# Kernel optimization log

Hardware: AMD Instinct MI355X
Metric: run time of the kernel (lower is better)

Reference implementation:

```python
import jax, jax.numpy as jnp
import numpy as np

DIM = 256      # z feature dim
HEADS = 8
C = 64         # per-head dim == x channel dim
INNER = HEADS * C  # 512


def setup_inputs() -> dict:
    key = jax.random.key(0)
    ks = jax.random.split(key, 8)
    b, h, w, m = 8, 64, 64, 256
    x = jax.random.normal(ks[0], (b, C, h, w), dtype=jnp.float32)
    z = jax.random.normal(ks[1], (b, m, DIM), dtype=jnp.float32)
    s = 1.0 / np.sqrt(DIM)
    Wk = jax.random.normal(ks[2], (DIM, INNER), dtype=jnp.float32) * s
    bk = jnp.zeros((INNER,), dtype=jnp.float32)
    Wv = jax.random.normal(ks[3], (DIM, INNER), dtype=jnp.float32) * s
    bv = jnp.zeros((INNER,), dtype=jnp.float32)
    Wo = jax.random.normal(ks[4], (INNER, C), dtype=jnp.float32) * (1.0 / np.sqrt(INNER))
    bo = jnp.zeros((C,), dtype=jnp.float32)
    return {"x": x, "z": z, "Wk": Wk, "bk": bk, "Wv": Wv, "bv": bv, "Wo": Wo, "bo": bo}


def reference(x, z, Wk, bk, Wv, bv, Wo, bo):
    b, c, h, w = x.shape
    m = z.shape[1]
    heads = Wk.shape[1] // c
    hw = h * w
    # Faithful to torch: raw view (b,c,h,w)->(b,hw,c), then repeat along feature
    # dim and raw view into (b, heads, hw, c).
    q = jnp.tile(x.reshape(b, hw, c), (1, 1, heads)).reshape(b, heads, hw, c)
    # k/v: Linear then raw view (b, m, heads*c) -> (b, heads, m, c).
    k = (z @ Wk + bk).reshape(b, heads, m, c)
    v = (z @ Wv + bv).reshape(b, heads, m, c)
    scale = c ** (-0.5)
    dots = jnp.einsum('bhlc,bhmc->bhlm', q, k) * scale
    attn = jax.nn.softmax(dots, axis=-1)
    out = jnp.einsum('bhlm,bhmc->bhlc', attn, v)
    out = jnp.transpose(out, (0, 2, 1, 3)).reshape(b, hw, heads * c)  # b l (h c)
    out = out @ Wo + bo  # (b, hw, c)
    # Faithful raw view back to (b, c, h, w), then residual.
    return x + out.reshape(b, c, h, w)
```

## Files before the change

kernel.cpp:

```cpp
#include <hip/hip_runtime.h>

#define HEADS 8
#define CH    64
#define HW    4096
#define MTOK  256
#define DIMZ  256
#define INNER 512
#define LROWS 512

typedef __attribute__((ext_vector_type(8))) __bf16 bf16x8;
typedef __attribute__((ext_vector_type(4))) float  f32x4;

__device__ __forceinline__ unsigned f2bf(float f) {
  unsigned u = __float_as_uint(f);
  return (u + 0x7fffu + ((u >> 16) & 1u)) >> 16;
}

__device__ __forceinline__ bf16x8 ld_bf8(const unsigned short* p) {
  uint4 v = *(const uint4*)p;
  return __builtin_bit_cast(bf16x8, v);
}

__device__ __forceinline__ bf16x8 cvt8(const float* p) {
  float4 f0 = *(const float4*)p;
  float4 f1 = *(const float4*)(p + 4);
  uint4 u;
  u.x = f2bf(f0.x) | (f2bf(f0.y) << 16);
  u.y = f2bf(f0.z) | (f2bf(f0.w) << 16);
  u.z = f2bf(f1.x) | (f2bf(f1.y) << 16);
  u.w = f2bf(f1.z) | (f2bf(f1.w) << 16);
  return __builtin_bit_cast(bf16x8, u);
}

__global__ __launch_bounds__(256) void kv_gen(
    const float* __restrict__ z,
    const float* __restrict__ Wk, const float* __restrict__ bk,
    const float* __restrict__ Wv, const float* __restrict__ bv,
    const float* __restrict__ Wo,
    unsigned short* __restrict__ klin, unsigned short* __restrict__ vt,
    unsigned short* __restrict__ WoT) {
  __shared__ unsigned short Tw[2][64][40];
  __shared__ float Tf[64][65];
  const int t = threadIdx.x;
  const int bn = blockIdx.y;

  if (bn == 16) {
    if (blockIdx.x >= 8) return;
    const int k0 = blockIdx.x * 64;
    const int rr = t >> 6, cc = t & 63;
#pragma unroll
    for (int it = 0; it < 16; ++it) {
      int r = it * 4 + rr;
      Tf[r][cc] = Wo[(size_t)(k0 + r) * CH + cc];
    }
    __syncthreads();
    const int nr = t >> 5, kp = t & 31;
#pragma unroll
    for (int it = 0; it < 8; ++it) {
      int n = it * 8 + nr;
      unsigned w = f2bf(Tf[kp * 2][n]) | (f2bf(Tf[kp * 2 + 1][n]) << 16);
      *(unsigned*)(WoT + (size_t)n * INNER + k0 + kp * 2) = w;
    }
    return;
  }

  const int lane = t & 63, wid = t >> 6;
  const int c = lane & 15, g = lane >> 4;
  const int mb = blockIdx.x;
  const bool isK = bn < 8;
  const int nb = bn & 7;
  const float* __restrict__ W    = isK ? Wk : Wv;
  const float* __restrict__ bias = isK ? bk : bv;
  const int m0 = mb * 64 + (wid >> 1) * 32;
  const int n0 = nb * 64 + (wid & 1) * 32;
  const int nloc = (wid & 1) * 32;
  const int skk = t >> 3, snn = (t & 7) * 8;

  f32x4 acc[2][2];
#pragma unroll
  for (int i = 0; i < 2; ++i)
#pragma unroll
    for (int j = 0; j < 2; ++j) acc[i][j] = (f32x4)0.f;

  {
    const float* wp = W + (size_t)skk * INNER + nb * 64 + snn;
    float4 w0 = *(const float4*)wp;
    float4 w1 = *(const float4*)(wp + 4);
    Tw[0][snn + 0][skk] = (unsigned short)f2bf(w0.x);
    Tw[0][snn + 1][skk] = (unsigned short)f2bf(w0.y);
    Tw[0][snn + 2][skk] = (unsigned short)f2bf(w0.z);
    Tw[0][snn + 3][skk] = (unsigned short)f2bf(w0.w);
    Tw[0][snn + 4][skk] = (unsigned short)f2bf(w1.x);
    Tw[0][snn + 5][skk] = (unsigned short)f2bf(w1.y);
    Tw[0][snn + 6][skk] = (unsigned short)f2bf(w1.z);
    Tw[0][snn + 7][skk] = (unsigned short)f2bf(w1.w);
  }
  __syncthreads();

#pragma unroll
  for (int s = 0; s < 8; ++s) {
    const int k0 = s * 32;
    if (s < 7) {
      const int nb2 = (s + 1) & 1;
      const float* wp = W + (size_t)(k0 + 32 + skk) * INNER + nb * 64 + snn;
      float4 w0 = *(const float4*)wp;
      float4 w1 = *(const float4*)(wp + 4);
      Tw[nb2][snn + 0][skk] = (unsigned short)f2bf(w0.x);
      Tw[nb2][snn + 1][skk] = (unsigned short)f2bf(w0.y);
      Tw[nb2][snn + 2][skk] = (unsigned short)f2bf(w0.z);
      Tw[nb2][snn + 3][skk] = (unsigned short)f2bf(w0.w);
      Tw[nb2][snn + 4][skk] = (unsigned short)f2bf(w1.x);
      Tw[nb2][snn + 5][skk] = (unsigned short)f2bf(w1.y);
      Tw[nb2][snn + 6][skk] = (unsigned short)f2bf(w1.z);
      Tw[nb2][snn + 7][skk] = (unsigned short)f2bf(w1.w);
    }
    const int cb = s & 1;
    bf16x8 a0 = cvt8(z + (size_t)(m0 + c) * DIMZ + k0 + 8 * g);
    bf16x8 a1 = cvt8(z + (size_t)(m0 + 16 + c) * DIMZ + k0 + 8 * g);
    bf16x8 b0 = *(const bf16x8*)&Tw[cb][nloc + c][8 * g];
    bf16x8 b1 = *(const bf16x8*)&Tw[cb][nloc + 16 + c][8 * g];
    if (isK) {
      acc[0][0] = __builtin_amdgcn_mfma_f32_16x16x32_bf16(b0, a0, acc[0][0], 0, 0, 0);
      acc[0][1] = __builtin_amdgcn_mfma_f32_16x16x32_bf16(b1, a0, acc[0][1], 0, 0, 0);
      acc[1][0] = __builtin_amdgcn_mfma_f32_16x16x32_bf16(b0, a1, acc[1][0], 0, 0, 0);
      acc[1][1] = __builtin_amdgcn_mfma_f32_16x16x32_bf16(b1, a1, acc[1][1], 0, 0, 0);
    } else {
      acc[0][0] = __builtin_amdgcn_mfma_f32_16x16x32_bf16(a0, b0, acc[0][0], 0, 0, 0);
      acc[0][1] = __builtin_amdgcn_mfma_f32_16x16x32_bf16(a0, b1, acc[0][1], 0, 0, 0);
      acc[1][0] = __builtin_amdgcn_mfma_f32_16x16x32_bf16(a1, b0, acc[1][0], 0, 0, 0);
      acc[1][1] = __builtin_amdgcn_mfma_f32_16x16x32_bf16(a1, b1, acc[1][1], 0, 0, 0);
    }
    __syncthreads();
  }

  if (isK) {
#pragma unroll
    for (int mt = 0; mt < 2; ++mt)
#pragma unroll
      for (int nt = 0; nt < 2; ++nt) {
        const int m = m0 + mt * 16 + c;
        const int n = n0 + nt * 16 + 4 * g;
        float4 b4 = *(const float4*)(bias + n);
        uint2 w;
        w.x = f2bf(acc[mt][nt][0] + b4.x) | (f2bf(acc[mt][nt][1] + b4.y) << 16);
        w.y = f2bf(acc[mt][nt][2] + b4.z) | (f2bf(acc[mt][nt][3] + b4.w) << 16);
        *(uint2*)(klin + (size_t)m * INNER + n) = w;
      }
  } else {
#pragma unroll
    for (int mt = 0; mt < 2; ++mt)
#pragma unroll
      for (int nt = 0; nt < 2; ++nt) {
        const int n = n0 + nt * 16 + c;
        const float bn1 = bias[n];
        const int m = m0 + mt * 16 + 4 * g;
        const int bb = m >> 8;
        const int mtk = m & 255;
        const int h = mtk >> 5, t0 = mtk & 31;
        const int cc2 = n & 63, cb2 = n >> 6;
        uint2 w;
        w.x = f2bf(acc[mt][nt][0] + bn1) | (f2bf(acc[mt][nt][1] + bn1) << 16);
        w.y = f2bf(acc[mt][nt][2] + bn1) | (f2bf(acc[mt][nt][3] + bn1) << 16);
        *(uint2*)(vt + ((size_t)((bb * HEADS + h) * CH + cc2)) * MTOK + cb2 * 32 + t0) = w;
      }
  }
}

__global__ __launch_bounds__(512) void attnproj(
    const float* __restrict__ x,
    const unsigned short* __restrict__ kbf,
    const unsigned short* __restrict__ vtbf,
    const unsigned short* __restrict__ WoT, const float* __restrict__ bo,
    float* __restrict__ y) {
  __shared__ __align__(16) char lds[65536 + 16384];
  char* Osh = lds + 65536;
  float* Sp = (float*)lds;
  const int t = threadIdx.x;
  const int lane = t & 63, wid = t >> 6;
  const int c = lane & 15, g = lane >> 4;
  const int bid = blockIdx.x;
  const int qc = bid & 31, b = bid >> 5;
  const int hh = wid;
  const int qbase = qc * 16;
  char* Pb = lds + wid * 8192;

  {
    const float* xs = x + (size_t)b * (HW * CH) + (size_t)hh * (LROWS * CH);
    const unsigned short* Kg = kbf + ((size_t)b * MTOK + hh * 32) * INNER;
    const unsigned short* Vg = vtbf + (size_t)(b * HEADS + hh) * (CH * MTOK);

    const float qs = 0.125f * 1.44269504089f;
    bf16x8 qfr[2];
#pragma unroll
    for (int ks = 0; ks < 2; ++ks) {
      const float* qp = xs + (size_t)(qbase + c) * CH + 32 * ks + 8 * g;
      float4 f0 = *(const float4*)qp;
      float4 f1 = *(const float4*)(qp + 4);
      uint4 u;
      u.x = f2bf(f0.x * qs) | (f2bf(f0.y * qs) << 16);
      u.y = f2bf(f0.z * qs) | (f2bf(f0.w * qs) << 16);
      u.z = f2bf(f1.x * qs) | (f2bf(f1.y * qs) << 16);
      u.w = f2bf(f1.z * qs) | (f2bf(f1.w * qs) << 16);
      qfr[ks] = __builtin_bit_cast(bf16x8, u);
    }

    f32x4 acc[16];
#pragma unroll
    for (int kf = 0; kf < 16; ++kf) acc[kf] = (f32x4)0.f;
#pragma unroll
    for (int kf = 0; kf < 16; ++kf) {
      const unsigned short* kp =
          Kg + (size_t)((kf & 1) * 16 + c) * INNER + (kf >> 1) * 64 + 8 * g;
      bf16x8 a0 = ld_bf8(kp);
      bf16x8 a1 = ld_bf8(kp + 32);
      acc[kf] = __builtin_amdgcn_mfma_f32_16x16x32_bf16(a0, qfr[0], acc[kf], 0, 0, 0);
      acc[kf] = __builtin_amdgcn_mfma_f32_16x16x32_bf16(a1, qfr[1], acc[kf], 0, 0, 0);
    }

    uint4 vpre[4][4];
#pragma unroll
    for (int ks = 0; ks < 4; ++ks)
#pragma unroll
      for (int cf = 0; cf < 4; ++cf)
        vpre[ks][cf] =
            *(const uint4*)(Vg + (size_t)(16 * cf + c) * MTOK + 32 * ks + 8 * g);

    float m = acc[0][0];
#pragma unroll
    for (int kf = 0; kf < 16; ++kf)
      m = fmaxf(m, fmaxf(fmaxf(acc[kf][0], acc[kf][1]),
                         fmaxf(acc[kf][2], acc[kf][3])));
    m = fmaxf(m, __shfl_xor(m, 16));
    m = fmaxf(m, __shfl_xor(m, 32));
    float sum = 0.f;
    const int rowb = c * 512;
#pragma unroll
    for (int kf = 0; kf < 16; ++kf) {
      float e0 = exp2f(acc[kf][0] - m);
      float e1 = exp2f(acc[kf][1] - m);
      float e2 = exp2f(acc[kf][2] - m);
      float e3 = exp2f(acc[kf][3] - m);
      sum += (e0 + e1) + (e2 + e3);
      uint2 w;
      w.x = f2bf(e0) | (f2bf(e1) << 16);
      w.y = f2bf(e2) | (f2bf(e3) << 16);
      *(uint2*)(Pb + ((rowb + (16 * kf + 4 * g) * 2) ^ ((c & 7) << 4))) = w;
    }
    sum += __shfl_xor(sum, 16);
    sum += __shfl_xor(sum, 32);
    const float inv = 1.f / sum;
    asm volatile("" ::: "memory");

    f32x4 o[4];
#pragma unroll
    for (int cf = 0; cf < 4; ++cf) o[cf] = (f32x4)0.f;
#pragma unroll
    for (int ks = 0; ks < 8; ++ks) {
      bf16x8 p = __builtin_bit_cast(bf16x8,
          *(const uint4*)(Pb + ((c * 512 + (32 * ks + 8 * g) * 2) ^ ((c & 7) << 4))));
#pragma unroll
      for (int cf = 0; cf < 4; ++cf) {
        bf16x8 a = (ks < 4)
            ? __builtin_bit_cast(bf16x8, vpre[ks][cf])
            : ld_bf8(Vg + (size_t)(16 * cf + c) * MTOK + 32 * ks + 8 * g);
        o[cf] = __builtin_amdgcn_mfma_f32_16x16x32_bf16(a, p, o[cf], 0, 0, 0);
      }
    }

#pragma unroll
    for (int cf = 0; cf < 4; ++cf) {
      f32x4 r = o[cf] * inv;
      uint2 w;
      w.x = f2bf(r[0]) | (f2bf(r[1]) << 16);
      w.y = f2bf(r[2]) | (f2bf(r[3]) << 16);
      int off = (c * 1024 + (hh * 64 + 16 * cf + 4 * g) * 2) ^ ((c & 7) << 4);
      *(uint2*)(Osh + off) = w;
    }
  }
  __syncthreads();

  {
    const int kw = wid * 64;
    f32x4 acc[4];
#pragma unroll
    for (int nt = 0; nt < 4; ++nt) acc[nt] = (f32x4)0.f;
#pragma unroll
    for (int s = 0; s < 2; ++s) {
      const int k0 = kw + s * 32;
      bf16x8 bfr = __builtin_bit_cast(bf16x8,
          *(const uint4*)(Osh + ((c * 1024 + (k0 + 8 * g) * 2) ^ ((c & 7) << 4))));
#pragma unroll
      for (int nt = 0; nt < 4; ++nt) {
        bf16x8 afr = ld_bf8(WoT + (size_t)(nt * 16 + c) * INNER + k0 + 8 * g);
        acc[nt] = __builtin_amdgcn_mfma_f32_16x16x32_bf16(afr, bfr, acc[nt], 0, 0, 0);
      }
    }
#pragma unroll
    for (int nt = 0; nt < 4; ++nt)
      *(f32x4*)&Sp[(wid * 16 + c) * 68 + nt * 16 + 4 * g] = acc[nt];
  }
  __syncthreads();

  const int i = t >> 5, jj = t & 31;
  const int j0 = (jj & 15) * 4, rh = jj >> 4;
  float4 b4 = *(const float4*)(bo + j0);
  float4 o4 = b4;
#pragma unroll
  for (int w = 0; w < 8; ++w) {
    float4 s = *(const float4*)&Sp[(w * 16 + i) * 68 + j0];
    o4.x += s.x; o4.y += s.y; o4.z += s.z; o4.w += s.w;
  }
  const int L = qbase + i;
  const float* xr = x + (size_t)b * (HW * CH) + (size_t)L * 8 * CH + j0;
  float*       yr = y + (size_t)b * (HW * CH) + (size_t)L * 8 * CH + j0;
#pragma unroll
  for (int r = 0; r < 4; ++r) {
    const int rr = rh * 4 + r;
    float4 xv = *(const float4*)(xr + rr * CH);
    float4 ov = make_float4(o4.x + xv.x, o4.y + xv.y, o4.z + xv.z, o4.w + xv.w);
    *(float4*)(yr + rr * CH) = ov;
  }
}

extern "C" void kernel_launch(void* const* d_in, const int* in_sizes, int n_in,
                              void* d_out, int out_size, void* d_ws, size_t ws_size,
                              hipStream_t stream) {
  const float* x  = (const float*)d_in[0];
  const float* z  = (const float*)d_in[1];
  const float* Wk = (const float*)d_in[2];
  const float* bk = (const float*)d_in[3];
  const float* Wv = (const float*)d_in[4];
  const float* bv = (const float*)d_in[5];
  const float* Wo = (const float*)d_in[6];
  const float* bo = (const float*)d_in[7];
  float* y = (float*)d_out;

  unsigned short* klin = (unsigned short*)d_ws;
  unsigned short* vt   = klin + (size_t)2048 * INNER;
  unsigned short* WoT  = vt   + (size_t)2048 * INNER;

  kv_gen<<<dim3(32, 17), 256, 0, stream>>>(z, Wk, bk, Wv, bv, Wo, klin, vt, WoT);
  attnproj<<<256, 512, 0, stream>>>(x, klin, vt, WoT, bo, y);
}
```

Before: 41.35 us.

## Fuse KV projection and attention into one cooperative kernel with grid sync

Merges the kv_gen and attnproj kernels into a single cooperative launch of 256 blocks. Each 512-thread block runs two 256-thread KV-projection tiles, and four blocks also transpose Wo, before a grid-wide sync. The block then goes straight into attention and the output projection, which removes the second launch and the gap between kernels. The residual x loads are also hoisted ahead of the projection barrier. In exchange it adds a grid barrier and relies on all 256 blocks being co-resident, which the 80KB of LDS per block may limit.

```diff
diff --git a/kernel.cpp b/kernel.cpp
--- a/kernel.cpp
+++ b/kernel.cpp
@@ -1,4 +1,7 @@
 #include <hip/hip_runtime.h>
+#include <hip/hip_cooperative_groups.h>
+
+namespace cg = cooperative_groups;
 
 #define HEADS 8
 #define CH    64
@@ -32,153 +35,145 @@
   return __builtin_bit_cast(bf16x8, u);
 }
 
-__global__ __launch_bounds__(256) void kv_gen(
-    const float* __restrict__ z,
+__global__ __launch_bounds__(512) void fused_all(
+    const float* __restrict__ x, const float* __restrict__ z,
     const float* __restrict__ Wk, const float* __restrict__ bk,
     const float* __restrict__ Wv, const float* __restrict__ bv,
-    const float* __restrict__ Wo,
+    const float* __restrict__ Wo, const float* __restrict__ bo,
     unsigned short* __restrict__ klin, unsigned short* __restrict__ vt,
-    unsigned short* __restrict__ WoT) {
-  __shared__ unsigned short Tw[2][64][40];
-  __shared__ float Tf[64][65];
+    unsigned short* __restrict__ WoT, float* __restrict__ y) {
+  __shared__ __align__(16) char lds[81920];
   const int t = threadIdx.x;
-  const int bn = blockIdx.y;
-
-  if (bn == 16) {
-    if (blockIdx.x >= 8) return;
-    const int k0 = blockIdx.x * 64;
-    const int rr = t >> 6, cc = t & 63;
-#pragma unroll
-    for (int it = 0; it < 16; ++it) {
-      int r = it * 4 + rr;
-      Tf[r][cc] = Wo[(size_t)(k0 + r) * CH + cc];
+  const int bid = blockIdx.x;
+
+  {
+    const int half = t >> 8, ht = t & 255;
+    const int vb = bid * 2 + half;
+    const int mb = vb >> 4, bn = vb & 15;
+    const bool isK = bn < 8;
+    const int nb = bn & 7;
+    const float* __restrict__ W    = isK ? Wk : Wv;
+    const float* __restrict__ bias = isK ? bk : bv;
+    const int lane = ht & 63, wid4 = ht >> 6;
+    const int c = lane & 15, g = lane >> 4;
+    const int m0 = mb * 64 + (wid4 >> 1) * 32;
+    const int n0 = nb * 64 + (wid4 & 1) * 32;
+    const int nloc = (wid4 & 1) * 32;
+    const int skk = ht >> 3, snn = (ht & 7) * 8;
+    unsigned short* Tw = (unsigned short*)(lds + half * 10240);
+    #define TW(buf, n, k) Tw[((buf) * 64 + (n)) * 40 + (k)]
+
+    f32x4 acc[2][2];
+#pragma unroll
+    for (int i = 0; i < 2; ++i)
+#pragma unroll
+      for (int j = 0; j < 2; ++j) acc[i][j] = (f32x4)0.f;
+
+    {
+      const float* wp = W + (size_t)skk * INNER + nb * 64 + snn;
+      float4 w0 = *(const float4*)wp;
+      float4 w1 = *(const float4*)(wp + 4);
+      TW(0, snn + 0, skk) = (unsigned short)f2bf(w0.x);
+      TW(0, snn + 1, skk) = (unsigned short)f2bf(w0.y);
+      TW(0, snn + 2, skk) = (unsigned short)f2bf(w0.z);
+      TW(0, snn + 3, skk) = (unsigned short)f2bf(w0.w);
+      TW(0, snn + 4, skk) = (unsigned short)f2bf(w1.x);
+      TW(0, snn + 5, skk) = (unsigned short)f2bf(w1.y);
+      TW(0, snn + 6, skk) = (unsigned short)f2bf(w1.z);
+      TW(0, snn + 7, skk) = (unsigned short)f2bf(w1.w);
     }
     __syncthreads();
-    const int nr = t >> 5, kp = t & 31;
-#pragma unroll
-    for (int it = 0; it < 8; ++it) {
-      int n = it * 8 + nr;
-      unsigned w = f2bf(Tf[kp * 2][n]) | (f2bf(Tf[kp * 2 + 1][n]) << 16);
-      *(unsigned*)(WoT + (size_t)n * INNER + k0 + kp * 2) = w;
-    }
-    return;
-  }
-
+
+#pragma unroll
+    for (int s = 0; s < 8; ++s) {
+      const int k0 = s * 32;
+      if (s < 7) {
+        const int nb2 = (s + 1) & 1;
+        const float* wp = W + (size_t)(k0 + 32 + skk) * INNER + nb * 64 + snn;
+        float4 w0 = *(const float4*)wp;
+        float4 w1 = *(const float4*)(wp + 4);
+        TW(nb2, snn + 0, skk) = (unsigned short)f2bf(w0.x);
+        TW(nb2, snn + 1, skk) = (unsigned short)f2bf(w0.y);
+        TW(nb2, snn + 2, skk) = (unsigned short)f2bf(w0.z);
+        TW(nb2, snn + 3, skk) = (unsigned short)f2bf(w0.w);
+        TW(nb2, snn + 4, skk) = (unsigned short)f2bf(w1.x);
+        TW(nb2, snn + 5, skk) = (unsigned short)f2bf(w1.y);
+        TW(nb2, snn + 6, skk) = (unsigned short)f2bf(w1.z);
+        TW(nb2, snn + 7, skk) = (unsigned short)f2bf(w1.w);
+      }
+      const int cbuf = s & 1;
+      bf16x8 a0 = cvt8(z + (size_t)(m0 + c) * DIMZ + k0 + 8 * g);
+      bf16x8 a1 = cvt8(z + (size_t)(m0 + 16 + c) * DIMZ + k0 + 8 * g);
+      bf16x8 b0 = *(const bf16x8*)&TW(cbuf, nloc + c, 8 * g);
+      bf16x8 b1 = *(const bf16x8*)&TW(cbuf, nloc + 16 + c, 8 * g);
+      if (isK) {
+        acc[0][0] = __builtin_amdgcn_mfma_f32_16x16x32_bf16(b0, a0, acc[0][0], 0, 0, 0);
+        acc[0][1] = __builtin_amdgcn_mfma_f32_16x16x32_bf16(b1, a0, acc[0][1], 0, 0, 0);
+        acc[1][0] = __builtin_amdgcn_mfma_f32_16x16x32_bf16(b0, a1, acc[1][0], 0, 0, 0);
+        acc[1][1] = __builtin_amdgcn_mfma_f32_16x16x32_bf16(b1, a1, acc[1][1], 0, 0, 0);
+      } else {
+        acc[0][0] = __builtin_amdgcn_mfma_f32_16x16x32_bf16(a0, b0, acc[0][0], 0, 0, 0);
+        acc[0][1] = __builtin_amdgcn_mfma_f32_16x16x32_bf16(a0, b1, acc[0][1], 0, 0, 0);
+        acc[1][0] = __builtin_amdgcn_mfma_f32_16x16x32_bf16(a1, b0, acc[1][0], 0, 0, 0);
+        acc[1][1] = __builtin_amdgcn_mfma_f32_16x16x32_bf16(a1, b1, acc[1][1], 0, 0, 0);
+      }
+      __syncthreads();
+    }
+    #undef TW
+
+    if (isK) {
+#pragma unroll
+      for (int mt = 0; mt < 2; ++mt)
+#pragma unroll
+        for (int nt = 0; nt < 2; ++nt) {
+          const int m = m0 + mt * 16 + c;
+          const int n = n0 + nt * 16 + 4 * g;
+          float4 b4 = *(const float4*)(bias + n);
+          uint2 w;
+          w.x = f2bf(acc[mt][nt][0] + b4.x) | (f2bf(acc[mt][nt][1] + b4.y) << 16);
+          w.y = f2bf(acc[mt][nt][2] + b4.z) | (f2bf(acc[mt][nt][3] + b4.w) << 16);
+          *(uint2*)(klin + (size_t)m * INNER + n) = w;
+        }
+    } else {
+#pragma unroll
+      for (int mt = 0; mt < 2; ++mt)
+#pragma unroll
+        for (int nt = 0; nt < 2; ++nt) {
+          const int n = n0 + nt * 16 + c;
+          const float bn1 = bias[n];
+          const int m = m0 + mt * 16 + 4 * g;
+          const int bb = m >> 8;
+          const int mtk = m & 255;
+          const int h = mtk >> 5, t0 = mtk & 31;
+          const int cc2 = n & 63, cb2 = n >> 6;
+          uint2 w;
+          w.x = f2bf(acc[mt][nt][0] + bn1) | (f2bf(acc[mt][nt][1] + bn1) << 16);
+          w.y = f2bf(acc[mt][nt][2] + bn1) | (f2bf(acc[mt][nt][3] + bn1) << 16);
+          *(uint2*)(vt + ((size_t)((bb * HEADS + h) * CH + cc2)) * MTOK + cb2 * 32 + t0) = w;
+        }
+    }
+  }
+
+  if (bid >= 252) {
+    const int idx0 = (bid - 252) * 512 + t;
+#pragma unroll
+    for (int it = 0; it < 4; ++it) {
+      int gidx = idx0 + it * 2048;
+      int n = gidx >> 7, k0 = (gidx & 127) * 4;
+      uint2 w;
+      w.x = f2bf(Wo[(size_t)k0 * CH + n])       | (f2bf(Wo[(size_t)(k0 + 1) * CH + n]) << 16);
+      w.y = f2bf(Wo[(size_t)(k0 + 2) * CH + n]) | (f2bf(Wo[(size_t)(k0 + 3) * CH + n]) << 16);
+      *(uint2*)(WoT + (size_t)n * INNER + k0) = w;
+    }
+  }
+
+  __threadfence();
+  cg::this_grid().sync();
+
+  char* Osh = lds + 65536;
+  float* Sp = (float*)lds;
   const int lane = t & 63, wid = t >> 6;
   const int c = lane & 15, g = lane >> 4;
-  const int mb = blockIdx.x;
-  const bool isK = bn < 8;
-  const int nb = bn & 7;
-  const float* __restrict__ W    = isK ? Wk : Wv;
-  const float* __restrict__ bias = isK ? bk : bv;
-  const int m0 = mb * 64 + (wid >> 1) * 32;
-  const int n0 = nb * 64 + (wid & 1) * 32;
-  const int nloc = (wid & 1) * 32;
-  const int skk = t >> 3, snn = (t & 7) * 8;
-
-  f32x4 acc[2][2];
-#pragma unroll
-  for (int i = 0; i < 2; ++i)
-#pragma unroll
-    for (int j = 0; j < 2; ++j) acc[i][j] = (f32x4)0.f;
-
-  {
-    const float* wp = W + (size_t)skk * INNER + nb * 64 + snn;
-    float4 w0 = *(const float4*)wp;
-    float4 w1 = *(const float4*)(wp + 4);
-    Tw[0][snn + 0][skk] = (unsigned short)f2bf(w0.x);
-    Tw[0][snn + 1][skk] = (unsigned short)f2bf(w0.y);
-    Tw[0][snn + 2][skk] = (unsigned short)f2bf(w0.z);
-    Tw[0][snn + 3][skk] = (unsigned short)f2bf(w0.w);
-    Tw[0][snn + 4][skk] = (unsigned short)f2bf(w1.x);
-    Tw[0][snn + 5][skk] = (unsigned short)f2bf(w1.y);
-    Tw[0][snn + 6][skk] = (unsigned short)f2bf(w1.z);
-    Tw[0][snn + 7][skk] = (unsigned short)f2bf(w1.w);
-  }
-  __syncthreads();
-
-#pragma unroll
-  for (int s = 0; s < 8; ++s) {
-    const int k0 = s * 32;
-    if (s < 7) {
-      const int nb2 = (s + 1) & 1;
-      const float* wp = W + (size_t)(k0 + 32 + skk) * INNER + nb * 64 + snn;
-      float4 w0 = *(const float4*)wp;
-      float4 w1 = *(const float4*)(wp + 4);
-      Tw[nb2][snn + 0][skk] = (unsigned short)f2bf(w0.x);
-      Tw[nb2][snn + 1][skk] = (unsigned short)f2bf(w0.y);
-      Tw[nb2][snn + 2][skk] = (unsigned short)f2bf(w0.z);
-      Tw[nb2][snn + 3][skk] = (unsigned short)f2bf(w0.w);
-      Tw[nb2][snn + 4][skk] = (unsigned short)f2bf(w1.x);
-      Tw[nb2][snn + 5][skk] = (unsigned short)f2bf(w1.y);
-      Tw[nb2][snn + 6][skk] = (unsigned short)f2bf(w1.z);
-      Tw[nb2][snn + 7][skk] = (unsigned short)f2bf(w1.w);
-    }
-    const int cb = s & 1;
-    bf16x8 a0 = cvt8(z + (size_t)(m0 + c) * DIMZ + k0 + 8 * g);
-    bf16x8 a1 = cvt8(z + (size_t)(m0 + 16 + c) * DIMZ + k0 + 8 * g);
-    bf16x8 b0 = *(const bf16x8*)&Tw[cb][nloc + c][8 * g];
-    bf16x8 b1 = *(const bf16x8*)&Tw[cb][nloc + 16 + c][8 * g];
-    if (isK) {
-      acc[0][0] = __builtin_amdgcn_mfma_f32_16x16x32_bf16(b0, a0, acc[0][0], 0, 0, 0);
-      acc[0][1] = __builtin_amdgcn_mfma_f32_16x16x32_bf16(b1, a0, acc[0][1], 0, 0, 0);
-      acc[1][0] = __builtin_amdgcn_mfma_f32_16x16x32_bf16(b0, a1, acc[1][0], 0, 0, 0);
-      acc[1][1] = __builtin_amdgcn_mfma_f32_16x16x32_bf16(b1, a1, acc[1][1], 0, 0, 0);
-    } else {
-      acc[0][0] = __builtin_amdgcn_mfma_f32_16x16x32_bf16(a0, b0, acc[0][0], 0, 0, 0);
-      acc[0][1] = __builtin_amdgcn_mfma_f32_16x16x32_bf16(a0, b1, acc[0][1], 0, 0, 0);
-      acc[1][0] = __builtin_amdgcn_mfma_f32_16x16x32_bf16(a1, b0, acc[1][0], 0, 0, 0);
-      acc[1][1] = __builtin_amdgcn_mfma_f32_16x16x32_bf16(a1, b1, acc[1][1], 0, 0, 0);
-    }
-    __syncthreads();
-  }
-
-  if (isK) {
-#pragma unroll
-    for (int mt = 0; mt < 2; ++mt)
-#pragma unroll
-      for (int nt = 0; nt < 2; ++nt) {
-        const int m = m0 + mt * 16 + c;
-        const int n = n0 + nt * 16 + 4 * g;
-        float4 b4 = *(const float4*)(bias + n);
-        uint2 w;
-        w.x = f2bf(acc[mt][nt][0] + b4.x) | (f2bf(acc[mt][nt][1] + b4.y) << 16);
-        w.y = f2bf(acc[mt][nt][2] + b4.z) | (f2bf(acc[mt][nt][3] + b4.w) << 16);
-        *(uint2*)(klin + (size_t)m * INNER + n) = w;
-      }
-  } else {
-#pragma unroll
-    for (int mt = 0; mt < 2; ++mt)
-#pragma unroll
-      for (int nt = 0; nt < 2; ++nt) {
-        const int n = n0 + nt * 16 + c;
-        const float bn1 = bias[n];
-        const int m = m0 + mt * 16 + 4 * g;
-        const int bb = m >> 8;
-        const int mtk = m & 255;
-        const int h = mtk >> 5, t0 = mtk & 31;
-        const int cc2 = n & 63, cb2 = n >> 6;
-        uint2 w;
-        w.x = f2bf(acc[mt][nt][0] + bn1) | (f2bf(acc[mt][nt][1] + bn1) << 16);
-        w.y = f2bf(acc[mt][nt][2] + bn1) | (f2bf(acc[mt][nt][3] + bn1) << 16);
-        *(uint2*)(vt + ((size_t)((bb * HEADS + h) * CH + cc2)) * MTOK + cb2 * 32 + t0) = w;
-      }
-  }
-}
-
-__global__ __launch_bounds__(512) void attnproj(
-    const float* __restrict__ x,
-    const unsigned short* __restrict__ kbf,
-    const unsigned short* __restrict__ vtbf,
-    const unsigned short* __restrict__ WoT, const float* __restrict__ bo,
-    float* __restrict__ y) {
-  __shared__ __align__(16) char lds[65536 + 16384];
-  char* Osh = lds + 65536;
-  float* Sp = (float*)lds;
-  const int t = threadIdx.x;
-  const int lane = t & 63, wid = t >> 6;
-  const int c = lane & 15, g = lane >> 4;
-  const int bid = blockIdx.x;
   const int qc = bid & 31, b = bid >> 5;
   const int hh = wid;
   const int qbase = qc * 16;
@@ -186,8 +181,8 @@
 
   {
     const float* xs = x + (size_t)b * (HW * CH) + (size_t)hh * (LROWS * CH);
-    const unsigned short* Kg = kbf + ((size_t)b * MTOK + hh * 32) * INNER;
-    const unsigned short* Vg = vtbf + (size_t)(b * HEADS + hh) * (CH * MTOK);
+    const unsigned short* Kg = klin + ((size_t)b * MTOK + hh * 32) * INNER;
+    const unsigned short* Vg = vt + (size_t)(b * HEADS + hh) * (CH * MTOK);
 
     const float qs = 0.125f * 1.44269504089f;
     bf16x8 qfr[2];
@@ -277,6 +272,15 @@
       *(uint2*)(Osh + off) = w;
     }
   }
+
+  const int ei = t >> 5, ejj = t & 31;
+  const int ej0 = (ejj & 15) * 4, erh = ejj >> 4;
+  const int eL = qbase + ei;
+  const float* xr = x + (size_t)b * (HW * CH) + (size_t)eL * 8 * CH + ej0;
+  float4 xv[4];
+#pragma unroll
+  for (int r = 0; r < 4; ++r) xv[r] = *(const float4*)(xr + (erh * 4 + r) * CH);
+
   __syncthreads();
 
   {
@@ -301,24 +305,19 @@
   }
   __syncthreads();
 
-  const int i = t >> 5, jj = t & 31;
-  const int j0 = (jj & 15) * 4, rh = jj >> 4;
-  float4 b4 = *(const float4*)(bo + j0);
+  float4 b4 = *(const float4*)(bo + ej0);
   float4 o4 = b4;
 #pragma unroll
   for (int w = 0; w < 8; ++w) {
-    float4 s = *(const float4*)&Sp[(w * 16 + i) * 68 + j0];
+    float4 s = *(const float4*)&Sp[(w * 16 + ei) * 68 + ej0];
     o4.x += s.x; o4.y += s.y; o4.z += s.z; o4.w += s.w;
   }
-  const int L = qbase + i;
-  const float* xr = x + (size_t)b * (HW * CH) + (size_t)L * 8 * CH + j0;
-  float*       yr = y + (size_t)b * (HW * CH) + (size_t)L * 8 * CH + j0;
+  float* yr = y + (size_t)b * (HW * CH) + (size_t)eL * 8 * CH + ej0;
 #pragma unroll
   for (int r = 0; r < 4; ++r) {
-    const int rr = rh * 4 + r;
-    float4 xv = *(const float4*)(xr + rr * CH);
-    float4 ov = make_float4(o4.x + xv.x, o4.y + xv.y, o4.z + xv.z, o4.w + xv.w);
-    *(float4*)(yr + rr * CH) = ov;
+    float4 ov = make_float4(o4.x + xv[r].x, o4.y + xv[r].y,
+                            o4.z + xv[r].z, o4.w + xv[r].w);
+    *(float4*)(yr + (erh * 4 + r) * CH) = ov;
   }
 }
 
@@ -339,6 +338,8 @@
   unsigned short* vt   = klin + (size_t)2048 * INNER;
   unsigned short* WoT  = vt   + (size_t)2048 * INNER;
 
-  kv_gen<<<dim3(32, 17), 256, 0, stream>>>(z, Wk, bk, Wv, bv, Wo, klin, vt, WoT);
-  attnproj<<<256, 512, 0, stream>>>(x, klin, vt, WoT, bo, y);
-}
+  void* args[12] = {&x, &z, &Wk, &bk, &Wv, &bv, &Wo, &bo,
+                    &klin, &vt, &WoT, &y};
+  hipLaunchCooperativeKernel((const void*)fused_all, dim3(256), dim3(512),
+                             args, 0, stream);
+}
```

Result: slower. 150.0 us (+262.7%).
